# Kernel tuning notes

Hardware: AMD Instinct MI355X
Metric: run time of the kernel (lower is better)

Reference implementation:

```python
import jax, jax.numpy as jnp
import numpy as np

B, N, E, D = 8, 10000, 160000, 256
H = D // 2
SLOPE = 0.2  # LeakyReLU negative slope


def setup_inputs() -> dict:
    key = jax.random.key(0)
    ks = jax.random.split(key, 8)
    node_feats = jax.random.normal(ks[0], (B, N, D), dtype=jnp.float32)
    edge_attr = jax.random.uniform(ks[1], (E, 1), dtype=jnp.float32)
    W1 = jax.random.normal(ks[2], (2 * D, H), dtype=jnp.float32) * 0.05
    b1 = jnp.zeros((H,), dtype=jnp.float32)
    W2 = jax.random.normal(ks[3], (H, 1), dtype=jnp.float32) * 0.05
    b2 = jnp.zeros((1,), dtype=jnp.float32)
    edge_index = jax.random.randint(ks[4], (2, E), 0, N, dtype=jnp.int64)
    valid_masks = jax.random.randint(ks[5], (B, N), 0, 2).astype(bool)
    return {"node_feats": node_feats, "edge_attr": edge_attr, "W1": W1, "b1": b1,
            "W2": W2, "b2": b2, "edge_index": edge_index, "valid_masks": valid_masks}


def reference(node_feats, edge_attr, W1, b1, W2, b2, edge_index, valid_masks):
    # node_feats: [B,N,D]; edge_index: [2,E] shared across batch
    d = node_feats.shape[-1]
    src, dst = edge_index[0], edge_index[1]
    # cat([src_feats, dst_feats]) @ W1 == src @ W1[:d] + dst @ W1[d:]
    # Project per-node first, then gather per-edge: avoids the [B,E,2D] concat.
    ps = jnp.einsum('bnd,dh->bnh', node_feats, W1[:d])   # [B,N,H]
    pd = jnp.einsum('bnd,dh->bnh', node_feats, W1[d:])   # [B,N,H]
    h = ps[:, src] + pd[:, dst] + b1                      # [B,E,H]
    h = jnp.where(h >= 0, h, SLOPE * h)                   # LeakyReLU(0.2)
    scores = jnp.einsum('beh,h->be', h, W2[:, 0]) + b2[0]  # [B,E]
    scores = scores * edge_attr[:, 0]                     # edge_attr multiplies pre-softmax
    w = jax.nn.softmax(scores, axis=1)                    # global softmax over all edges
    # sparse_coo(edge_index, w) @ node_feats: out[src[e]] += w[e] * feats[dst[e]]
    msg = w[..., None] * node_feats[:, dst]               # [B,E,D]
    n = node_feats.shape[1]
    agg = jax.vmap(lambda m: jax.ops.segment_sum(m, src, num_segments=n))(msg)  # [B,N,D]
    mask = valid_masks.astype(node_feats.dtype)           # [B,N]
    cnt = mask.sum(axis=1)                                # [B]
    masked_mean = (agg * mask[..., None]).sum(axis=1) / jnp.maximum(cnt, 1.0)[:, None]
    full_mean = agg.mean(axis=1)
    graph_feats = jnp.where((cnt > 0)[:, None], masked_mean, full_mean)  # [B,D]
    return graph_feats, w
```

## Files before the change

### kernel.cpp

```cpp
#include <hip/hip_runtime.h>
#include <hip/hip_bf16.h>
#include <hip/hip_fp16.h>

#define B_ 8
#define N_ 10000
#define E_ 160000
#define D_ 256
#define H_ 128
#define SLOPE 0.2f
#define NCHUNK 200

#define NB_ 256
#define EPB_ (E_ / NB_)
#define BINS_ 256
#define NPB_ (N_ / 16)
#define SUBS_ 16

#define SB_ 256
#define SEB_ (E_ / SB_)

typedef __attribute__((ext_vector_type(8))) _Float16 v8h;
typedef __attribute__((ext_vector_type(4))) _Float16 v4h;
typedef __attribute__((ext_vector_type(2))) _Float16 v2h;
typedef __attribute__((ext_vector_type(4))) float f32x4;

static __device__ __forceinline__ float dot2f(v2h a, v2h b, float c) {
#if __has_builtin(__builtin_amdgcn_fdot2)
    return __builtin_amdgcn_fdot2(a, b, c, false);
#else
    return fmaf((float)a.y, (float)b.y, fmaf((float)a.x, (float)b.x, c));
#endif
}

__global__ __launch_bounds__(64) void k_detect(const int* __restrict__ eidx_raw,
                                               const unsigned int* __restrict__ mask32,
                                               int* __restrict__ flags) {
    const int t = threadIdx.x;
    unsigned long long oddnz = __ballot(eidx_raw[2 * t + 1] != 0);
    unsigned long long mgt1  = __ballot(mask32[t] > 1u);
    if (t == 0) {
        flags[0] = (oddnz == 0ull) ? 1 : 0;
        flags[1] = (mgt1 != 0ull) ? 1 : 0;
    }
}

__global__ __launch_bounds__(256) void k_canon(const int* __restrict__ eidx_raw,
                                               const unsigned char* __restrict__ mask8,
                                               const unsigned int* __restrict__ mask32,
                                               const int* __restrict__ flags,
                                               const float* __restrict__ W1,
                                               const float* __restrict__ b1,
                                               const float* __restrict__ W2,
                                               int* __restrict__ ce,
                                               unsigned char* __restrict__ cm,
                                               unsigned char* __restrict__ cmT,
                                               __half* __restrict__ Wt,
                                               __half* __restrict__ b1h,
                                               __half* __restrict__ w2h) {
    const int i = blockIdx.x * 256 + threadIdx.x;
    const int f_e = flags[0], f_m = flags[1];
    if (i < 2 * E_) ce[i] = f_e ? eidx_raw[2 * i] : eidx_raw[i];
    if (i < B_ * N_) {
        unsigned char v = f_m ? (unsigned char)(mask8[i] != 0)
                              : (unsigned char)(mask32[i] != 0u);
        cm[i] = v;
        const int b = i / N_;
        const int n = i - b * N_;
        cmT[n * 8 + b] = v;
    }
    if (i < 2 * 256 * 128) {
        const int f = i & 127;
        const int row = i >> 7;
        const int c = row >> 8, k = row & 255;
        Wt[((c * 128 + f) * 256) + k] = __float2half(W1[row * 128 + f]);
    }
    if (i < 128) {
        b1h[i] = __float2half(b1[i]);
        w2h[i] = __float2half(W2[i]);
    }
}

__global__ __launch_bounds__(256) void khist(const int* __restrict__ ce,
                                             const unsigned char* __restrict__ cm,
                                             int* __restrict__ hpart,
                                             float* __restrict__ cnt) {
    const int tid = threadIdx.x;
    if (blockIdx.x < NB_) {
        __shared__ int h[BINS_];
        h[tid] = 0;
        __syncthreads();
        const int base = blockIdx.x * EPB_;
        for (int i = tid; i < EPB_; i += 256) {
            const int s = ce[base + i], d = ce[E_ + base + i];
            const int bin = (d / NPB_) * 16 + s / NPB_;
            atomicAdd(&h[bin], 1);
        }
        __syncthreads();
        hpart[blockIdx.x * BINS_ + tid] = h[tid];
    } else {
        const int b = blockIdx.x - NB_;
        int c = 0;
        for (int i = tid; i < N_; i += 256) c += cm[b * N_ + i] ? 1 : 0;
        __shared__ int red[256];
        red[tid] = c;
        __syncthreads();
        for (int s = 128; s > 0; s >>= 1) {
            if (tid < s) red[tid] += red[tid + s];
            __syncthreads();
        }
        if (tid == 0) cnt[b] = (float)red[0];
    }
}

__global__ __launch_bounds__(256) void kprefix(const int* __restrict__ hpart,
                                               int* __restrict__ offsetG,
                                               int* __restrict__ bstart) {
    __shared__ int cnt[BINS_];
    __shared__ int excl[BINS_];
    const int bin = threadIdx.x;
    int c = 0;
    for (int b = 0; b < NB_; b++) c += hpart[b * BINS_ + bin];
    cnt[bin] = c;
    __syncthreads();
    if (bin == 0) {
        int r = 0;
        for (int i = 0; i < BINS_; i++) { excl[i] = r; r += cnt[i]; }
    }
    __syncthreads();
    if ((bin & 15) == 0) bstart[bin >> 4] = excl[bin];
    if (bin == 0) bstart[16] = E_;
    int run = excl[bin];
    for (int b = 0; b < NB_; b++) {
        offsetG[b * BINS_ + bin] = run;
        run += hpart[b * BINS_ + bin];
    }
}

__global__ __launch_bounds__(256) void kscatter(const int* __restrict__ ce,
                                                const int* __restrict__ offsetG,
                                                int4* __restrict__ esort,
                                                int* __restrict__ rank) {
    __shared__ int loc[BINS_];
    const int tid = threadIdx.x;
    loc[tid] = offsetG[blockIdx.x * BINS_ + tid];
    __syncthreads();
    const int base = blockIdx.x * EPB_;
    for (int i = tid; i < EPB_; i += 256) {
        const int e = base + i;
        const int s = ce[e], d = ce[E_ + e];
        const int bin = (d / NPB_) * 16 + s / NPB_;
        const int pos = atomicAdd(&loc[bin], 1);
        esort[pos] = make_int4(s, d, e, 0);
        rank[e] = pos;
    }
}

__global__ __launch_bounds__(256) void k1_mfma(const float* __restrict__ X,
                                               const __half* __restrict__ Wt,
                                               __half* __restrict__ ps,
                                               __half* __restrict__ pd) {
    const int rb = blockIdx.x;
    const int tid = threadIdx.x;
    const int wave = tid >> 6, lane = tid & 63;
    const int quad = lane >> 4, l16 = lane & 15;

    __shared__ __align__(16) char smem[64 * 136 * 2];
    _Float16* Xs = (_Float16*)smem;
    _Float16* T  = (_Float16*)smem;

    f32x4 acc[2][2][4];
#pragma unroll
    for (int c = 0; c < 2; c++)
#pragma unroll
        for (int i = 0; i < 2; i++)
#pragma unroll
            for (int j = 0; j < 4; j++) acc[c][i][j] = (f32x4){0.f, 0.f, 0.f, 0.f};

    const int row_base = rb * 64;
    const int sr = tid >> 3;
    const int sc = (tid & 7) * 4;

    const float* xsrc  = &X[(size_t)(row_base + sr) * 256 + sc];
    const float* xsrc2 = xsrc + 32 * 256;
    const __half* wbase = &Wt[((size_t)(wave * 32 + l16)) * 256 + quad * 8];

    float4 xa, xb;
    v8h wcur[2][2], wnxt[2][2];

    xa = *(const float4*)(xsrc);
    xb = *(const float4*)(xsrc2);
#pragma unroll
    for (int cb = 0; cb < 2; cb++)
#pragma unroll
        for (int ft = 0; ft < 2; ft++)
            wcur[cb][ft] = *(const v8h*)(wbase + (size_t)(cb * 128 + ft * 16) * 256);
    {
        v4h pa = {(_Float16)xa.x, (_Float16)xa.y, (_Float16)xa.z, (_Float16)xa.w};
        v4h pb = {(_Float16)xb.x, (_Float16)xb.y, (_Float16)xb.z, (_Float16)xb.w};
        *(v4h*)&Xs[sr * 40 + sc] = pa;
        *(v4h*)&Xs[(sr + 32) * 40 + sc] = pb;
    }
    __syncthreads();

    for (int kc = 0; kc < 8; ++kc) {
        const int cur = kc & 1;
        if (kc < 7) {
            xa = *(const float4*)(xsrc + (kc + 1) * 32);
            xb = *(const float4*)(xsrc2 + (kc + 1) * 32);
#pragma unroll
            for (int cb = 0; cb < 2; cb++)
#pragma unroll
                for (int ft = 0; ft < 2; ft++)
                    wnxt[cb][ft] = *(const v8h*)(wbase + (size_t)(cb * 128 + ft * 16) * 256 + (kc + 1) * 32);
        }
#pragma unroll
        for (int nt = 0; nt < 4; ++nt) {
            v8h xf = *(v8h*)&Xs[cur * (64 * 40) + (nt * 16 + l16) * 40 + quad * 8];
            acc[0][0][nt] = __builtin_amdgcn_mfma_f32_16x16x32_f16(wcur[0][0], xf, acc[0][0][nt], 0, 0, 0);
            acc[0][1][nt] = __builtin_amdgcn_mfma_f32_16x16x32_f16(wcur[0][1], xf, acc[0][1][nt], 0, 0, 0);
            acc[1][0][nt] = __builtin_amdgcn_mfma_f32_16x16x32_f16(wcur[1][0], xf, acc[1][0][nt], 0, 0, 0);
            acc[1][1][nt] = __builtin_amdgcn_mfma_f32_16x16x32_f16(wcur[1][1], xf, acc[1][1][nt], 0, 0, 0);
        }
        if (kc < 7) {
            const int nb = (cur ^ 1) * (64 * 40);
            v4h pa = {(_Float16)xa.x, (_Float16)xa.y, (_Float16)xa.z, (_Float16)xa.w};
            v4h pb = {(_Float16)xb.x, (_Float16)xb.y, (_Float16)xb.z, (_Float16)xb.w};
            *(v4h*)&Xs[nb + sr * 40 + sc] = pa;
            *(v4h*)&Xs[nb + (sr + 32) * 40 + sc] = pb;
#pragma unroll
            for (int cb = 0; cb < 2; cb++)
#pragma unroll
                for (int ft = 0; ft < 2; ft++)
                    wcur[cb][ft] = wnxt[cb][ft];
        }
        __syncthreads();
    }

#pragma unroll
    for (int cb = 0; cb < 2; ++cb) {
        if (cb) __syncthreads();
#pragma unroll
        for (int nt = 0; nt < 4; ++nt)
#pragma unroll
            for (int ft = 0; ft < 2; ++ft) {
                f32x4 a = acc[cb][ft][nt];
                v4h h = {(_Float16)a.x, (_Float16)a.y, (_Float16)a.z, (_Float16)a.w};
                *(v4h*)&T[(nt * 16 + l16) * 136 + wave * 32 + ft * 16 + quad * 4] = h;
            }
        __syncthreads();
        __half* outp = cb ? pd : ps;
#pragma unroll
        for (int pass = 0; pass < 4; ++pass) {
            const int r = pass * 16 + (tid >> 4);
            const int f8 = (tid & 15) * 8;
            const int R = row_base + r;
            const int b = R / N_;
            const int n = R - b * N_;
            *(float4*)(outp + ((size_t)(n * 8 + b)) * 128 + f8) =
                *(const float4*)&T[r * 136 + f8];
        }
    }
}

__global__ __launch_bounds__(256) void k2_scores(const __half* __restrict__ ps,
                                                 const __half* __restrict__ pd,
                                                 const int4* __restrict__ esort,
                                                 const __half* __restrict__ b1h,
                                                 const __half* __restrict__ w2h,
                                                 const float* __restrict__ b2,
                                                 const float* __restrict__ eattr,
                                                 float* __restrict__ scS) {
    const int tid = threadIdx.x;
    const int wave = tid >> 6;
    const int lane = tid & 63;
    const int bid = blockIdx.x;
    const int lb = (bid & 7) * 2500 + (bid >> 3);
    const int e0 = lb * 8 + wave * 2;

    const int b = lane >> 3;
    const int hi = (lane & 7) * 16;

    v2h b1p[8], w2p[8];
    {
        const v2h* bp = (const v2h*)(b1h + hi);
        const v2h* wp = (const v2h*)(w2h + hi);
#pragma unroll
        for (int j = 0; j < 8; j++) { b1p[j] = bp[j]; w2p[j] = wp[j]; }
    }
    const float bias2 = b2[0];
    const v2h slp = {(_Float16)SLOPE, (_Float16)SLOPE};

#pragma unroll
    for (int q = 0; q < 2; q++) {
        const int e = e0 + q;
        const int4 er = esort[e];
        const int src = er.x, dst = er.y, orig = er.z;

        const float4* aps = (const float4*)&ps[((size_t)src * 8 + b) * 128 + hi];
        const float4* apd = (const float4*)&pd[((size_t)dst * 8 + b) * 128 + hi];
        float4 rs[2] = {aps[0], aps[1]};
        float4 rd[2] = {apd[0], apd[1]};
        const v2h* sv = (const v2h*)rs;
        const v2h* dv = (const v2h*)rd;

        float acc = 0.f;
#pragma unroll
        for (int j = 0; j < 8; j++) {
            v2h x = sv[j] + dv[j] + b1p[j];
            v2h l = __builtin_elementwise_max(x, x * slp);
            acc = dot2f(l, w2p[j], acc);
        }
        acc += __shfl_xor(acc, 1);
        acc += __shfl_xor(acc, 2);
        acc += __shfl_xor(acc, 4);

        if ((lane & 7) == 0) {
            scS[(size_t)e * 8 + b] = (acc + bias2) * eattr[orig];
        }
    }
}

__global__ __launch_bounds__(256) void k3s_stats(const float* __restrict__ scS,
                                                 float* __restrict__ pmax,
                                                 double* __restrict__ psum) {
    const int tid = threadIdx.x;
    const int wave = tid >> 6, lane = tid & 63;
    const int base = blockIdx.x * SEB_;

    float fm[8];
#pragma unroll
    for (int j = 0; j < 8; j++) fm[j] = -3.4e38f;
    for (int i = tid; i < SEB_; i += 256) {
        const float4* s4 = (const float4*)&scS[(size_t)(base + i) * 8];
        float4 a = s4[0], b = s4[1];
        fm[0] = fmaxf(fm[0], a.x); fm[1] = fmaxf(fm[1], a.y);
        fm[2] = fmaxf(fm[2], a.z); fm[3] = fmaxf(fm[3], a.w);
        fm[4] = fmaxf(fm[4], b.x); fm[5] = fmaxf(fm[5], b.y);
        fm[6] = fmaxf(fm[6], b.z); fm[7] = fmaxf(fm[7], b.w);
    }
#pragma unroll
    for (int k = 1; k <= 32; k <<= 1)
#pragma unroll
        for (int j = 0; j < 8; j++) fm[j] = fmaxf(fm[j], __shfl_xor(fm[j], k));
    __shared__ float lmax[4][8];
    if (lane == 0)
#pragma unroll
        for (int j = 0; j < 8; j++) lmax[wave][j] = fm[j];
    __syncthreads();
    float m[8];
#pragma unroll
    for (int j = 0; j < 8; j++)
        m[j] = fmaxf(fmaxf(lmax[0][j], lmax[1][j]), fmaxf(lmax[2][j], lmax[3][j]));

    double s[8];
#pragma unroll
    for (int j = 0; j < 8; j++) s[j] = 0.0;
    for (int i = tid; i < SEB_; i += 256) {
        const float4* s4 = (const float4*)&scS[(size_t)(base + i) * 8];
        float4 a = s4[0], b = s4[1];
        s[0] += (double)expf(a.x - m[0]); s[1] += (double)expf(a.y - m[1]);
        s[2] += (double)expf(a.z - m[2]); s[3] += (double)expf(a.w - m[3]);
        s[4] += (double)expf(b.x - m[4]); s[5] += (double)expf(b.y - m[5]);
        s[6] += (double)expf(b.z - m[6]); s[7] += (double)expf(b.w - m[7]);
    }
#pragma unroll
    for (int k = 1; k <= 32; k <<= 1)
#pragma unroll
        for (int j = 0; j < 8; j++) s[j] += __shfl_xor(s[j], k);
    __shared__ double lsum[4][8];
    if (lane == 0)
#pragma unroll
        for (int j = 0; j < 8; j++) lsum[wave][j] = s[j];
    __syncthreads();
    if (tid < 8) {
        pmax[blockIdx.x * 8 + tid] = m[tid];
        psum[blockIdx.x * 8 + tid] = lsum[0][tid] + lsum[1][tid] + lsum[2][tid] + lsum[3][tid];
    }
}

static __device__ __forceinline__ void stats_combine(const float* __restrict__ pmax,
                                                     const double* __restrict__ psum,
                                                     int tid, float* smx, float* sinvx) {
    if (tid < 64) {
        float mc[SB_ / 64][8];
        float v[8];
#pragma unroll
        for (int j = 0; j < 8; j++) v[j] = -3.4e38f;
#pragma unroll
        for (int g = 0; g < SB_ / 64; g++) {
            const float4* p4 = (const float4*)&pmax[(g * 64 + tid) * 8];
            float4 a = p4[0], b = p4[1];
            mc[g][0] = a.x; mc[g][1] = a.y; mc[g][2] = a.z; mc[g][3] = a.w;
            mc[g][4] = b.x; mc[g][5] = b.y; mc[g][6] = b.z; mc[g][7] = b.w;
#pragma unroll
            for (int j = 0; j < 8; j++) v[j] = fmaxf(v[j], mc[g][j]);
        }
#pragma unroll
        for (int k = 1; k <= 32; k <<= 1)
#pragma unroll
            for (int j = 0; j < 8; j++) v[j] = fmaxf(v[j], __shfl_xor(v[j], k));
        double z[8];
#pragma unroll
        for (int j = 0; j < 8; j++) z[j] = 0.0;
#pragma unroll
        for (int g = 0; g < SB_ / 64; g++)
#pragma unroll
            for (int j = 0; j < 8; j++)
                z[j] += psum[(g * 64 + tid) * 8 + j] * (double)expf(mc[g][j] - v[j]);
#pragma unroll
        for (int k = 1; k <= 32; k <<= 1)
#pragma unroll
            for (int j = 0; j < 8; j++) z[j] += __shfl_xor(z[j], k);
        if (tid == 0)
#pragma unroll
            for (int j = 0; j < 8; j++) { smx[j] = v[j]; sinvx[j] = (float)(1.0 / z[j]); }
    }
}

__global__ __launch_bounds__(256) void k3e_norm(const float* __restrict__ scS,
                                                const int* __restrict__ rank,
                                                const float* __restrict__ pmax,
                                                const double* __restrict__ psum,
                                                float* __restrict__ wout) {
    const int tid = threadIdx.x;
    __shared__ float smx[8], sinvx[8];
    stats_combine(pmax, psum, tid, smx, sinvx);
    __syncthreads();

    const int e = blockIdx.x * 256 + tid;
    const int p = rank[e];
    const float4* s4 = (const float4*)&scS[(size_t)p * 8];
    float4 a = s4[0], b = s4[1];
    float wv[8];
    wv[0] = expf(a.x - smx[0]) * sinvx[0]; wv[1] = expf(a.y - smx[1]) * sinvx[1];
    wv[2] = expf(a.z - smx[2]) * sinvx[2]; wv[3] = expf(a.w - smx[3]) * sinvx[3];
    wv[4] = expf(b.x - smx[4]) * sinvx[4]; wv[5] = expf(b.y - smx[5]) * sinvx[5];
    wv[6] = expf(b.z - smx[6]) * sinvx[6]; wv[7] = expf(b.w - smx[7]) * sinvx[7];
#pragma unroll
    for (int j = 0; j < 8; j++) wout[(size_t)j * E_ + e] = wv[j];
}

__global__ __launch_bounds__(256) void k3f_bin(const int4* __restrict__ esort,
                                               const float* __restrict__ scS,
                                               const unsigned char* __restrict__ cmT,
                                               const float* __restrict__ pmax,
                                               const double* __restrict__ psum,
                                               const int* __restrict__ bstart,
                                               float* __restrict__ Wpf,
                                               float* __restrict__ Wpm) {
    const int bucket = blockIdx.x;
    const int sub = blockIdx.y;
    const int tid = threadIdx.x;

    __shared__ float smx[8], sinvx[8];
    stats_combine(pmax, psum, tid, smx, sinvx);

    __shared__ float lWf[NPB_ * 8];
    __shared__ float lWm[NPB_ * 8];
    for (int i = tid; i < NPB_ * 8; i += 256) { lWf[i] = 0.f; lWm[i] = 0.f; }
    __syncthreads();

    float m[8], inv[8];
#pragma unroll
    for (int j = 0; j < 8; j++) { m[j] = smx[j]; inv[j] = sinvx[j]; }

    const int bs = bstart[bucket], be = bstart[bucket + 1];
    const int len = be - bs;
    const int s0 = bs + (int)((long long)len * sub / SUBS_);
    const int s1 = bs + (int)((long long)len * (sub + 1) / SUBS_);
    const int nbase = bucket * NPB_;

    for (int p = s0 + tid; p < s1; p += 256) {
        const int4 er = esort[p];
        const int src = er.x;
        const int rel = er.y - nbase;
        const float4* s4 = (const float4*)&scS[(size_t)p * 8];
        float4 a = s4[0], b = s4[1];
        float wv[8];
        wv[0] = expf(a.x - m[0]) * inv[0]; wv[1] = expf(a.y - m[1]) * inv[1];
        wv[2] = expf(a.z - m[2]) * inv[2]; wv[3] = expf(a.w - m[3]) * inv[3];
        wv[4] = expf(b.x - m[4]) * inv[4]; wv[5] = expf(b.y - m[5]) * inv[5];
        wv[6] = expf(b.z - m[6]) * inv[6]; wv[7] = expf(b.w - m[7]) * inv[7];
        const unsigned long long mm = *(const unsigned long long*)&cmT[src * 8];
        float* lf = &lWf[rel * 8];
        float* lm = &lWm[rel * 8];
#pragma unroll
        for (int j = 0; j < 8; j++) {
            atomicAdd(&lf[j], wv[j]);
            if ((mm >> (8 * j)) & 1ull) atomicAdd(&lm[j], wv[j]);
        }
    }
    __syncthreads();

    float* of = Wpf + ((size_t)bucket * SUBS_ + sub) * (NPB_ * 8);
    float* om = Wpm + ((size_t)bucket * SUBS_ + sub) * (NPB_ * 8);
    for (int i = tid; i < NPB_ * 8; i += 256) { of[i] = lWf[i]; om[i] = lWm[i]; }
}

__global__ __launch_bounds__(256) void k3g_reduce(const float* __restrict__ Wpf,
                                                  const float* __restrict__ Wpm,
                                                  float* __restrict__ WfT,
                                                  float* __restrict__ WmT) {
    const int i = blockIdx.x * 256 + threadIdx.x;
    if (i >= N_ * 8) return;
    const int n = i >> 3, b = i & 7;
    const int bucket = n / NPB_;
    const int rel = n - bucket * NPB_;
    float sf = 0.f, sm = 0.f;
#pragma unroll
    for (int sub = 0; sub < SUBS_; sub++) {
        const size_t off = ((size_t)bucket * SUBS_ + sub) * (NPB_ * 8) + rel * 8 + b;
        sf += Wpf[off];
        sm += Wpm[off];
    }
    WfT[i] = sf;
    WmT[i] = sm;
}

__global__ __launch_bounds__(256) void k4b_wsum(const float* __restrict__ X,
                                                const float* __restrict__ WmT,
                                                const float* __restrict__ WfT,
                                                float* __restrict__ gpart) {
    const int c = blockIdx.x;
    const int b = blockIdx.y;
    const int tx = threadIdx.x & 63;
    const int ty = threadIdx.x >> 6;
    const int npc = N_ / NCHUNK;
    const int n0 = c * npc;

    const float4* X4 = (const float4*)(X + (size_t)b * N_ * 256);
    float4 am = {0.f, 0.f, 0.f, 0.f};
    float4 af = {0.f, 0.f, 0.f, 0.f};

    for (int n = n0 + ty; n < n0 + npc; n += 4) {
        float wm = WmT[n * 8 + b];
        float wf = WfT[n * 8 + b];
        float4 v = X4[(size_t)n * 64 + tx];
        am.x = fmaf(wm, v.x, am.x); am.y = fmaf(wm, v.y, am.y);
        am.z = fmaf(wm, v.z, am.z); am.w = fmaf(wm, v.w, am.w);
        af.x = fmaf(wf, v.x, af.x); af.y = fmaf(wf, v.y, af.y);
        af.z = fmaf(wf, v.z, af.z); af.w = fmaf(wf, v.w, af.w);
    }

    __shared__ float4 red[256];
    red[threadIdx.x] = am;
    __syncthreads();
    if (ty == 0) {
        float4 r1 = red[tx + 64], r2 = red[tx + 128], r3 = red[tx + 192];
        am.x += r1.x + r2.x + r3.x; am.y += r1.y + r2.y + r3.y;
        am.z += r1.z + r2.z + r3.z; am.w += r1.w + r2.w + r3.w;
    }
    __syncthreads();
    red[threadIdx.x] = af;
    __syncthreads();
    if (ty == 0) {
        float4 r1 = red[tx + 64], r2 = red[tx + 128], r3 = red[tx + 192];
        af.x += r1.x + r2.x + r3.x; af.y += r1.y + r2.y + r3.y;
        af.z += r1.z + r2.z + r3.z; af.w += r1.w + r2.w + r3.w;
        float4* gp4 = (float4*)gpart;
        gp4[((c * 2 + 0) * 8 + b) * 64 + tx] = am;
        gp4[((c * 2 + 1) * 8 + b) * 64 + tx] = af;
    }
}

__global__ __launch_bounds__(256) void k5_final(const float* __restrict__ gpart,
                                                const float* __restrict__ cnt,
                                                float* __restrict__ gf) {
    const int b = blockIdx.x;
    const int d = threadIdx.x;
    float sm = 0.f, sf = 0.f;
    for (int c = 0; c < NCHUNK; c++) {
        sm += gpart[((c * 2 + 0) * 8 + b) * 256 + d];
        sf += gpart[((c * 2 + 1) * 8 + b) * 256 + d];
    }
    const float cn = cnt[b];
    gf[b * 256 + d] = (cn > 0.f) ? (sm / cn) : (sf / (float)N_);
}

static inline char* align16(char* p) {
    return (char*)(((uintptr_t)p + 15) & ~(uintptr_t)15);
}

extern "C" void kernel_launch(void* const* d_in, const int* in_sizes, int n_in,
                              void* d_out, int out_size, void* d_ws, size_t ws_size,
                              hipStream_t stream) {
    const float* X     = (const float*)d_in[0];
    const float* eattr = (const float*)d_in[1];
    const float* W1    = (const float*)d_in[2];
    const float* b1    = (const float*)d_in[3];
    const float* W2    = (const float*)d_in[4];
    const float* b2    = (const float*)d_in[5];
    const int*   eidx_raw = (const int*)d_in[6];
    const unsigned char* mask8 = (const unsigned char*)d_in[7];
    const unsigned int*  mask32 = (const unsigned int*)d_in[7];

    float* out  = (float*)d_out;
    float* gf   = out;
    float* wout = out + 2048;

    char* cur = (char*)d_ws;
    __half* ps_h = (__half*)cur;             cur += (size_t)N_ * 8 * 128 * 2;
    __half* pd_h = (__half*)cur;             cur += (size_t)N_ * 8 * 128 * 2;
    __half* Wt   = (__half*)cur;             cur += 2 * 128 * 256 * 2;
    int* ce      = (int*)cur;                cur += 2 * E_ * 4;
    unsigned char* cmT = (unsigned char*)cur; cur += N_ * 8;
    unsigned char* cm  = (unsigned char*)cur; cur += B_ * N_;
    cur = align16(cur);
    float* cnt   = (float*)cur;              cur += 8 * 4;
    int* flags   = (int*)cur;                cur += 2 * 4;
    cur = align16(cur);
    float* pmax  = (float*)cur;              cur += SB_ * 8 * 4;
    cur = align16(cur);
    double* psum = (double*)cur;             cur += SB_ * 8 * 8;
    float* gpart = (float*)cur;              cur += NCHUNK * 2 * 8 * 256 * 4;
    int* hpart   = (int*)cur;                cur += NB_ * BINS_ * 4;
    int* offsetG = (int*)cur;                cur += NB_ * BINS_ * 4;
    int* bstart  = (int*)cur;                cur += 32 * 4;
    cur = align16(cur);
    int4* esort  = (int4*)cur;               cur += (size_t)E_ * 16;
    int* rankB   = (int*)cur;                cur += E_ * 4;
    __half* b1h  = (__half*)cur;             cur += 128 * 2;
    __half* w2h  = (__half*)cur;             cur += 128 * 2;
    cur = align16(cur);
    float* scS   = (float*)cur;              cur += (size_t)E_ * 8 * 4;

    char* ocur = (char*)d_ws;
    float* Wpf = (float*)ocur;               ocur += (size_t)16 * SUBS_ * NPB_ * 8 * 4;
    float* Wpm = (float*)ocur;               ocur += (size_t)16 * SUBS_ * NPB_ * 8 * 4;
    float* WfT = (float*)ocur;               ocur += N_ * 8 * 4;
    float* WmT = (float*)ocur;               ocur += N_ * 8 * 4;

    hipLaunchKernelGGL(k_detect, dim3(1), dim3(64), 0, stream, eidx_raw, mask32, flags);
    hipLaunchKernelGGL(k_canon, dim3(1250), dim3(256), 0, stream,
                       eidx_raw, mask8, mask32, flags, W1, b1, W2,
                       ce, cm, cmT, Wt, b1h, w2h);
    hipLaunchKernelGGL(khist, dim3(NB_ + 8), dim3(256), 0, stream, ce, cm, hpart, cnt);
    hipLaunchKernelGGL(kprefix, dim3(1), dim3(256), 0, stream, hpart, offsetG, bstart);
    hipLaunchKernelGGL(kscatter, dim3(NB_), dim3(256), 0, stream, ce, offsetG, esort, rankB);
    hipLaunchKernelGGL(k1_mfma, dim3(1250), dim3(256), 0, stream, X, Wt, ps_h, pd_h);
    hipLaunchKernelGGL(k2_scores, dim3(E_ / 8), dim3(256), 0, stream,
                       ps_h, pd_h, esort, b1h, w2h, b2, eattr, scS);
    hipLaunchKernelGGL(k3s_stats, dim3(SB_), dim3(256), 0, stream, scS, pmax, psum);
    hipLaunchKernelGGL(k3e_norm, dim3(E_ / 256), dim3(256), 0, stream,
                       scS, rankB, pmax, psum, wout);
    hipLaunchKernelGGL(k3f_bin, dim3(16, SUBS_), dim3(256), 0, stream,
                       esort, scS, cmT, pmax, psum, bstart, Wpf, Wpm);
    hipLaunchKernelGGL(k3g_reduce, dim3((N_ * 8 + 255) / 256), dim3(256), 0, stream,
                       Wpf, Wpm, WfT, WmT);
    hipLaunchKernelGGL(k4b_wsum, dim3(NCHUNK, 8), dim3(256), 0, stream, X, WmT, WfT, gpart);
    hipLaunchKernelGGL(k5_final, dim3(8), dim3(256), 0, stream, gpart, cnt, gf);
}
```

Measured before the change: 294.8 us.

## Merge independent prep, scatter and softmax kernels into fewer launches

```diff
diff --git a/kernel.cpp b/kernel.cpp
--- a/kernel.cpp
+++ b/kernel.cpp
@@ -8,13 +8,13 @@
 #define D_ 256
 #define H_ 128
 #define SLOPE 0.2f
-#define NCHUNK 200
-
-#define NB_ 256
+#define NCHUNK 100
+
+#define NB_ 64
 #define EPB_ (E_ / NB_)
 #define BINS_ 256
 #define NPB_ (N_ / 16)
-#define SUBS_ 16
+#define SUBS_ 8
 
 #define SB_ 256
 #define SEB_ (E_ / SB_)
@@ -32,83 +32,76 @@
 #endif
 }
 
-__global__ __launch_bounds__(64) void k_detect(const int* __restrict__ eidx_raw,
-                                               const unsigned int* __restrict__ mask32,
-                                               int* __restrict__ flags) {
-    const int t = threadIdx.x;
-    unsigned long long oddnz = __ballot(eidx_raw[2 * t + 1] != 0);
-    unsigned long long mgt1  = __ballot(mask32[t] > 1u);
-    if (t == 0) {
-        flags[0] = (oddnz == 0ull) ? 1 : 0;
-        flags[1] = (mgt1 != 0ull) ? 1 : 0;
-    }
-}
-
-__global__ __launch_bounds__(256) void k_canon(const int* __restrict__ eidx_raw,
-                                               const unsigned char* __restrict__ mask8,
-                                               const unsigned int* __restrict__ mask32,
-                                               const int* __restrict__ flags,
-                                               const float* __restrict__ W1,
-                                               const float* __restrict__ b1,
-                                               const float* __restrict__ W2,
-                                               int* __restrict__ ce,
-                                               unsigned char* __restrict__ cm,
-                                               unsigned char* __restrict__ cmT,
-                                               __half* __restrict__ Wt,
-                                               __half* __restrict__ b1h,
-                                               __half* __restrict__ w2h) {
-    const int i = blockIdx.x * 256 + threadIdx.x;
-    const int f_e = flags[0], f_m = flags[1];
-    if (i < 2 * E_) ce[i] = f_e ? eidx_raw[2 * i] : eidx_raw[i];
-    if (i < B_ * N_) {
-        unsigned char v = f_m ? (unsigned char)(mask8[i] != 0)
-                              : (unsigned char)(mask32[i] != 0u);
-        cm[i] = v;
-        const int b = i / N_;
-        const int n = i - b * N_;
-        cmT[n * 8 + b] = v;
-    }
-    if (i < 2 * 256 * 128) {
-        const int f = i & 127;
-        const int row = i >> 7;
-        const int c = row >> 8, k = row & 255;
-        Wt[((c * 128 + f) * 256) + k] = __float2half(W1[row * 128 + f]);
-    }
-    if (i < 128) {
-        b1h[i] = __float2half(b1[i]);
-        w2h[i] = __float2half(W2[i]);
-    }
-}
-
-__global__ __launch_bounds__(256) void khist(const int* __restrict__ ce,
-                                             const unsigned char* __restrict__ cm,
-                                             int* __restrict__ hpart,
-                                             float* __restrict__ cnt) {
+static __device__ __forceinline__ void block_flags(const int* __restrict__ eidx_raw,
+                                                   const unsigned int* __restrict__ mask32,
+                                                   int tid, int* sfl) {
+    if (tid < 64) {
+        unsigned long long oddnz = __ballot(eidx_raw[2 * tid + 1] != 0);
+        unsigned long long mgt1  = __ballot(mask32[tid] > 1u);
+        if (tid == 0) {
+            sfl[0] = (oddnz == 0ull) ? 1 : 0;
+            sfl[1] = (mgt1 != 0ull) ? 1 : 0;
+        }
+    }
+    __syncthreads();
+}
+
+__global__ __launch_bounds__(256) void kprep(const int* __restrict__ eidx_raw,
+                                             const unsigned char* __restrict__ mask8,
+                                             const unsigned int* __restrict__ mask32,
+                                             const float* __restrict__ W1,
+                                             const float* __restrict__ b1,
+                                             const float* __restrict__ W2,
+                                             int* __restrict__ ce,
+                                             unsigned char* __restrict__ cmT,
+                                             __half* __restrict__ Wt,
+                                             __half* __restrict__ b1h,
+                                             __half* __restrict__ w2h,
+                                             int* __restrict__ cnti,
+                                             int* __restrict__ hpart) {
     const int tid = threadIdx.x;
-    if (blockIdx.x < NB_) {
+    __shared__ int sfl[2];
+
+    if (blockIdx.x < 1250) {
+        block_flags(eidx_raw, mask32, tid, sfl);
+        const int f_e = sfl[0], f_m = sfl[1];
+        const int i = blockIdx.x * 256 + tid;
+        if (i < 2 * E_) ce[i] = f_e ? eidx_raw[2 * i] : eidx_raw[i];
+        if (i < B_ * N_) {
+            unsigned char v = f_m ? (unsigned char)(mask8[i] != 0)
+                                  : (unsigned char)(mask32[i] != 0u);
+            const int b = i / N_;
+            const int n = i - b * N_;
+            cmT[n * 8 + b] = v;
+            if (v) atomicAdd(&cnti[b], 1);
+        }
+        if (i < 2 * 256 * 128) {
+            const int f = i & 127;
+            const int row = i >> 7;
+            const int c = row >> 8, k = row & 255;
+            Wt[((c * 128 + f) * 256) + k] = __float2half(W1[row * 128 + f]);
+        }
+        if (i < 128) {
+            b1h[i] = __float2half(b1[i]);
+            w2h[i] = __float2half(W2[i]);
+        }
+    } else {
+        block_flags(eidx_raw, mask32, tid, sfl);
+        const int f_e = sfl[0];
         __shared__ int h[BINS_];
         h[tid] = 0;
         __syncthreads();
-        const int base = blockIdx.x * EPB_;
+        const int hb = blockIdx.x - 1250;
+        const int base = hb * EPB_;
         for (int i = tid; i < EPB_; i += 256) {
-            const int s = ce[base + i], d = ce[E_ + base + i];
+            const int e = base + i;
+            const int s = f_e ? eidx_raw[2 * e] : eidx_raw[e];
+            const int d = f_e ? eidx_raw[2 * (E_ + e)] : eidx_raw[E_ + e];
             const int bin = (d / NPB_) * 16 + s / NPB_;
             atomicAdd(&h[bin], 1);
         }
         __syncthreads();
-        hpart[blockIdx.x * BINS_ + tid] = h[tid];
-    } else {
-        const int b = blockIdx.x - NB_;
-        int c = 0;
-        for (int i = tid; i < N_; i += 256) c += cm[b * N_ + i] ? 1 : 0;
-        __shared__ int red[256];
-        red[tid] = c;
-        __syncthreads();
-        for (int s = 128; s > 0; s >>= 1) {
-            if (tid < s) red[tid] += red[tid + s];
-            __syncthreads();
-        }
-        if (tid == 0) cnt[b] = (float)red[0];
+        hpart[hb * BINS_ + tid] = h[tid];
     }
 }
 
@@ -136,35 +129,37 @@
     }
 }
 
-__global__ __launch_bounds__(256) void kscatter(const int* __restrict__ ce,
-                                                const int* __restrict__ offsetG,
-                                                int4* __restrict__ esort,
-                                                int* __restrict__ rank) {
-    __shared__ int loc[BINS_];
-    const int tid = threadIdx.x;
-    loc[tid] = offsetG[blockIdx.x * BINS_ + tid];
-    __syncthreads();
-    const int base = blockIdx.x * EPB_;
-    for (int i = tid; i < EPB_; i += 256) {
-        const int e = base + i;
-        const int s = ce[e], d = ce[E_ + e];
-        const int bin = (d / NPB_) * 16 + s / NPB_;
-        const int pos = atomicAdd(&loc[bin], 1);
-        esort[pos] = make_int4(s, d, e, 0);
-        rank[e] = pos;
-    }
-}
-
 __global__ __launch_bounds__(256) void k1_mfma(const float* __restrict__ X,
                                                const __half* __restrict__ Wt,
                                                __half* __restrict__ ps,
-                                               __half* __restrict__ pd) {
+                                               __half* __restrict__ pd,
+                                               const int* __restrict__ ce,
+                                               const int* __restrict__ offsetG,
+                                               int4* __restrict__ esort,
+                                               int* __restrict__ rank) {
+    const int tid = threadIdx.x;
+    __shared__ __align__(16) char smem[64 * 136 * 2];
+
+    if (blockIdx.x >= 1250) {
+        int* loc = (int*)smem;
+        const int sb = blockIdx.x - 1250;
+        loc[tid] = offsetG[sb * BINS_ + tid];
+        __syncthreads();
+        const int base = sb * EPB_;
+        for (int i = tid; i < EPB_; i += 256) {
+            const int e = base + i;
+            const int s = ce[e], d = ce[E_ + e];
+            const int bin = (d / NPB_) * 16 + s / NPB_;
+            const int pos = atomicAdd(&loc[bin], 1);
+            esort[pos] = make_int4(s, d, e, 0);
+            rank[e] = pos;
+        }
+        return;
+    }
+
     const int rb = blockIdx.x;
-    const int tid = threadIdx.x;
     const int wave = tid >> 6, lane = tid & 63;
     const int quad = lane >> 4, l16 = lane & 15;
-
-    __shared__ __align__(16) char smem[64 * 136 * 2];
     _Float16* Xs = (_Float16*)smem;
     _Float16* T  = (_Float16*)smem;
 
@@ -417,46 +412,42 @@
     }
 }
 
-__global__ __launch_bounds__(256) void k3e_norm(const float* __restrict__ scS,
-                                                const int* __restrict__ rank,
-                                                const float* __restrict__ pmax,
-                                                const double* __restrict__ psum,
-                                                float* __restrict__ wout) {
+__global__ __launch_bounds__(256) void k3ef(const int4* __restrict__ esort,
+                                            const float* __restrict__ scS,
+                                            const unsigned char* __restrict__ cmT,
+                                            const float* __restrict__ pmax,
+                                            const double* __restrict__ psum,
+                                            const int* __restrict__ bstart,
+                                            const int* __restrict__ rank,
+                                            float* __restrict__ Wpf,
+                                            float* __restrict__ Wpm,
+                                            float* __restrict__ wout) {
     const int tid = threadIdx.x;
     __shared__ float smx[8], sinvx[8];
-    stats_combine(pmax, psum, tid, smx, sinvx);
-    __syncthreads();
-
-    const int e = blockIdx.x * 256 + tid;
-    const int p = rank[e];
-    const float4* s4 = (const float4*)&scS[(size_t)p * 8];
-    float4 a = s4[0], b = s4[1];
-    float wv[8];
-    wv[0] = expf(a.x - smx[0]) * sinvx[0]; wv[1] = expf(a.y - smx[1]) * sinvx[1];
-    wv[2] = expf(a.z - smx[2]) * sinvx[2]; wv[3] = expf(a.w - smx[3]) * sinvx[3];
-    wv[4] = expf(b.x - smx[4]) * sinvx[4]; wv[5] = expf(b.y - smx[5]) * sinvx[5];
-    wv[6] = expf(b.z - smx[6]) * sinvx[6]; wv[7] = expf(b.w - smx[7]) * sinvx[7];
-#pragma unroll
-    for (int j = 0; j < 8; j++) wout[(size_t)j * E_ + e] = wv[j];
-}
-
-__global__ __launch_bounds__(256) void k3f_bin(const int4* __restrict__ esort,
-                                               const float* __restrict__ scS,
-                                               const unsigned char* __restrict__ cmT,
-                                               const float* __restrict__ pmax,
-                                               const double* __restrict__ psum,
-                                               const int* __restrict__ bstart,
-                                               float* __restrict__ Wpf,
-                                               float* __restrict__ Wpm) {
-    const int bucket = blockIdx.x;
-    const int sub = blockIdx.y;
-    const int tid = threadIdx.x;
-
-    __shared__ float smx[8], sinvx[8];
-    stats_combine(pmax, psum, tid, smx, sinvx);
-
     __shared__ float lWf[NPB_ * 8];
     __shared__ float lWm[NPB_ * 8];
+
+    stats_combine(pmax, psum, tid, smx, sinvx);
+
+    if (blockIdx.x >= 16 * SUBS_) {
+        __syncthreads();
+        const int e = (blockIdx.x - 16 * SUBS_) * 256 + tid;
+        const int p = rank[e];
+        const float4* s4 = (const float4*)&scS[(size_t)p * 8];
+        float4 a = s4[0], b = s4[1];
+        float wv[8];
+        wv[0] = expf(a.x - smx[0]) * sinvx[0]; wv[1] = expf(a.y - smx[1]) * sinvx[1];
+        wv[2] = expf(a.z - smx[2]) * sinvx[2]; wv[3] = expf(a.w - smx[3]) * sinvx[3];
+        wv[4] = expf(b.x - smx[4]) * sinvx[4]; wv[5] = expf(b.y - smx[5]) * sinvx[5];
+        wv[6] = expf(b.z - smx[6]) * sinvx[6]; wv[7] = expf(b.w - smx[7]) * sinvx[7];
+#pragma unroll
+        for (int j = 0; j < 8; j++) wout[(size_t)j * E_ + e] = wv[j];
+        return;
+    }
+
+    const int bucket = blockIdx.x / SUBS_;
+    const int sub = blockIdx.x % SUBS_;
+
     for (int i = tid; i < NPB_ * 8; i += 256) { lWf[i] = 0.f; lWm[i] = 0.f; }
     __syncthreads();
 
@@ -564,7 +555,7 @@
 }
 
 __global__ __launch_bounds__(256) void k5_final(const float* __restrict__ gpart,
-                                                const float* __restrict__ cnt,
+                                                const int* __restrict__ cnti,
                                                 float* __restrict__ gf) {
     const int b = blockIdx.x;
     const int d = threadIdx.x;
@@ -573,7 +564,7 @@
         sm += gpart[((c * 2 + 0) * 8 + b) * 256 + d];
         sf += gpart[((c * 2 + 1) * 8 + b) * 256 + d];
     }
-    const float cn = cnt[b];
+    const float cn = (float)cnti[b];
     gf[b * 256 + d] = (cn > 0.f) ? (sm / cn) : (sf / (float)N_);
 }
 
@@ -604,10 +595,8 @@
     __half* Wt   = (__half*)cur;             cur += 2 * 128 * 256 * 2;
     int* ce      = (int*)cur;                cur += 2 * E_ * 4;
     unsigned char* cmT = (unsigned char*)cur; cur += N_ * 8;
-    unsigned char* cm  = (unsigned char*)cur; cur += B_ * N_;
     cur = align16(cur);
-    float* cnt   = (float*)cur;              cur += 8 * 4;
-    int* flags   = (int*)cur;                cur += 2 * 4;
+    int* cnti    = (int*)cur;                cur += 8 * 4;
     cur = align16(cur);
     float* pmax  = (float*)cur;              cur += SB_ * 8 * 4;
     cur = align16(cur);
@@ -630,23 +619,20 @@
     float* WfT = (float*)ocur;               ocur += N_ * 8 * 4;
     float* WmT = (float*)ocur;               ocur += N_ * 8 * 4;
 
-    hipLaunchKernelGGL(k_detect, dim3(1), dim3(64), 0, stream, eidx_raw, mask32, flags);
-    hipLaunchKernelGGL(k_canon, dim3(1250), dim3(256), 0, stream,
-                       eidx_raw, mask8, mask32, flags, W1, b1, W2,
-                       ce, cm, cmT, Wt, b1h, w2h);
-    hipLaunchKernelGGL(khist, dim3(NB_ + 8), dim3(256), 0, stream, ce, cm, hpart, cnt);
+    hipMemsetAsync(cnti, 0, 8 * sizeof(int), stream);
+    hipLaunchKernelGGL(kprep, dim3(1250 + NB_), dim3(256), 0, stream,
+                       eidx_raw, mask8, mask32, W1, b1, W2,
+                       ce, cmT, Wt, b1h, w2h, cnti, hpart);
     hipLaunchKernelGGL(kprefix, dim3(1), dim3(256), 0, stream, hpart, offsetG, bstart);
-    hipLaunchKernelGGL(kscatter, dim3(NB_), dim3(256), 0, stream, ce, offsetG, esort, rankB);
-    hipLaunchKernelGGL(k1_mfma, dim3(1250), dim3(256), 0, stream, X, Wt, ps_h, pd_h);
+    hipLaunchKernelGGL(k1_mfma, dim3(1250 + NB_), dim3(256), 0, stream,
+                       X, Wt, ps_h, pd_h, ce, offsetG, esort, rankB);
     hipLaunchKernelGGL(k2_scores, dim3(E_ / 8), dim3(256), 0, stream,
                        ps_h, pd_h, esort, b1h, w2h, b2, eattr, scS);
     hipLaunchKernelGGL(k3s_stats, dim3(SB_), dim3(256), 0, stream, scS, pmax, psum);
-    hipLaunchKernelGGL(k3e_norm, dim3(E_ / 256), dim3(256), 0, stream,
-                       scS, rankB, pmax, psum, wout);
-    hipLaunchKernelGGL(k3f_bin, dim3(16, SUBS_), dim3(256), 0, stream,
-                       esort, scS, cmT, pmax, psum, bstart, Wpf, Wpm);
+    hipLaunchKernelGGL(k3ef, dim3(16 * SUBS_ + E_ / 256), dim3(256), 0, stream,
+                       esort, scS, cmT, pmax, psum, bstart, rankB, Wpf, Wpm, wout);
     hipLaunchKernelGGL(k3g_reduce, dim3((N_ * 8 + 255) / 256), dim3(256), 0, stream,
                        Wpf, Wpm, WfT, WmT);
     hipLaunchKernelGGL(k4b_wsum, dim3(NCHUNK, 8), dim3(256), 0, stream, X, WmT, WfT, gpart);
-    hipLaunchKernelGGL(k5_final, dim3(8), dim3(256), 0, stream, gpart, cnt, gf);
-}
+    hipLaunchKernelGGL(k5_final, dim3(8), dim3(256), 0, stream, gpart, cnti, gf);
+}
```

Result: slower. 725.8 us (+146.2%).
